# Performance work log

Hardware: AMD Instinct MI355X
Metric: run time of the kernel (lower is better)

## Reference

```python
import jax, jax.numpy as jnp
import numpy as np

B, T, D, H, HF, L, NL = 8, 512, 1024, 16, 4096, 4, 128
HD = D // H  # head dim = 64


def rel_pos_embed(seq_len, dim):
    # Relative sinusoidal embeddings for positions -seq_len .. seq_len-1 (TENER / fairseq style)
    half = dim // 2
    freq = jnp.exp(jnp.arange(half, dtype=jnp.float32) * (-np.log(10000.0) / (half - 1)))
    pos = jnp.arange(-seq_len, seq_len, dtype=jnp.float32)[:, None] * freq[None, :]
    return jnp.concatenate([jnp.sin(pos), jnp.cos(pos)], axis=1)  # (2T, dim)


def layer_norm(x, g, b, eps=1e-5):
    m = jnp.mean(x, axis=-1, keepdims=True)
    v = jnp.mean((x - m) ** 2, axis=-1, keepdims=True)
    return (x - m) * jax.lax.rsqrt(v + eps) * g + b


def rel_attention(x, mask, qv_w, r_r, r_w, pos):
    # x: (B,T,D); qv_w: (D,2D); r_r,r_w: (H,HD); pos: (2T,HD)
    q, v = jnp.split(x @ qv_w, 2, axis=-1)
    q = q.reshape(B, T, H, HD).transpose(0, 2, 1, 3)  # bhqd
    k = x.reshape(B, T, H, HD).transpose(0, 2, 1, 3)  # key is raw input per head (TENER)
    v = v.reshape(B, T, H, HD).transpose(0, 2, 1, 3)
    AC = jnp.einsum('bhqd,bhkd->bhqk', q + r_r[:, None, :], k)
    # B term + D term over all 2T relative positions, then shift: BD[q,k] = BDf[q, T + k - q]
    BDf = jnp.einsum('bhqd,ld->bhql', q, pos) + jnp.einsum('hd,ld->hl', r_w, pos)[None, :, None, :]
    idx = T + jnp.arange(T)[None, :] - jnp.arange(T)[:, None]  # (T,T), values in [1, 2T-1]
    BD = jnp.take_along_axis(BDf, idx[None, None], axis=3)  # (B,H,T,T)
    scores = (AC + BD) / np.float32(np.sqrt(HD))
    scores = jnp.where(mask[:, None, None, :], scores, jnp.float32(-1e9))
    attn = jax.nn.softmax(scores, axis=-1)
    out = jnp.einsum('bhqk,bhkd->bhqd', attn, v)
    return out.transpose(0, 2, 1, 3).reshape(B, T, D)


def setup_inputs() -> dict:
    key = jax.random.key(0)
    ks = jax.random.split(key, 8)
    s = 0.02
    return {
        'x': jax.random.normal(ks[0], (B, T, D), jnp.float32),
        'mask': jnp.ones((B, T), dtype=bool),
        'qv_w': jax.random.normal(ks[1], (L, D, 2 * D), jnp.float32) * s,
        'r_r_bias': jax.random.normal(ks[2], (L, H, HD), jnp.float32) * s,
        'r_w_bias': jax.random.normal(ks[3], (L, H, HD), jnp.float32) * s,
        'ln1_g': jnp.ones((L, D), jnp.float32), 'ln1_b': jnp.zeros((L, D), jnp.float32),
        'w1': jax.random.normal(ks[4], (L, D, HF), jnp.float32) * s, 'b1': jnp.zeros((L, HF), jnp.float32),
        'w2': jax.random.normal(ks[5], (L, HF, D), jnp.float32) * s, 'b2': jnp.zeros((L, D), jnp.float32),
        'ln2_g': jnp.ones((L, D), jnp.float32), 'ln2_b': jnp.zeros((L, D), jnp.float32),
        'cls_w': jax.random.normal(ks[6], (D, NL), jnp.float32) * s, 'cls_b': jnp.zeros((NL,), jnp.float32),
    }


def reference(x, mask, qv_w, r_r_bias, r_w_bias, ln1_g, ln1_b, w1, b1, w2, b2, ln2_g, ln2_b, cls_w, cls_b):
    pos = rel_pos_embed(T, HD)  # (2T, HD)
    h = x
    for l in range(L):  # post-norm relative transformer layer
        h = layer_norm(h + rel_attention(h, mask, qv_w[l], r_r_bias[l], r_w_bias[l], pos), ln1_g[l], ln1_b[l])
        ff = jax.nn.leaky_relu(h @ w1[l] + b1[l]) @ w2[l] + b2[l]
        h = layer_norm(h + ff, ln2_g[l], ln2_b[l])
    return h @ cls_w + cls_b  # logits (B,T,NL)
```

## Files before the change

### kernel.cpp

```cpp
#include <hip/hip_runtime.h>
#include <math.h>

namespace {

constexpr int B = 8, T = 512, D = 1024, H = 16, HD = 64, HF = 4096, L = 4, NL = 128;

typedef _Float16 half8 __attribute__((ext_vector_type(8)));
typedef _Float16 half4 __attribute__((ext_vector_type(4)));
typedef float f32x4 __attribute__((ext_vector_type(4)));

__device__ __forceinline__ void gload16(const void* g, void* l) {
  __builtin_amdgcn_global_load_lds(
      (const __attribute__((address_space(1))) void*)g,
      (__attribute__((address_space(3))) void*)l, 16, 0, 0);
}

__device__ __forceinline__ void stage_half(const _Float16* g0,
                                           const _Float16* g1, char* dst) {
  gload16(g0, dst);
  gload16(g1, dst + 8192);
}

template <int OUT16, int ACT, int HASBIAS>
__global__ __launch_bounds__(256) void gemm_f16(
    const _Float16* __restrict__ A, const _Float16* __restrict__ Bt,
    const float* __restrict__ bias, void* __restrict__ Cout,
    int M, int N, int K) {
  (void)M;
  __shared__ __align__(16) _Float16 Alds[128 * 32];
  __shared__ __align__(16) _Float16 Blds[128 * 32];
  const int t = threadIdx.x;
  const int lane = t & 63;
  const int m0 = blockIdx.y * 128, n0 = blockIdx.x * 128;
  const int wm = (t >> 7) * 64;
  const int wn = ((t >> 6) & 1) * 64;
  f32x4 acc[4][4] = {};
  const int r0 = t >> 2, kc0 = (t & 3) * 8;
  const int r1 = (t + 256) >> 2, kc1 = (t & 3) * 8;
  _Float16* al0 = &Alds[(t & 192) * 8];
  _Float16* al1 = &Alds[(256 + (t & 192)) * 8];
  _Float16* bl0 = &Blds[(t & 192) * 8];
  _Float16* bl1 = &Blds[(256 + (t & 192)) * 8];
  const _Float16* Ar0 = A + (size_t)(m0 + r0) * K + kc0;
  const _Float16* Ar1 = A + (size_t)(m0 + r1) * K + kc1;
  const _Float16* Br0 = Bt + (size_t)(n0 + r0) * K + kc0;
  const _Float16* Br1 = Bt + (size_t)(n0 + r1) * K + kc1;
  const int ml = lane & 15, qd = lane >> 4;

  for (int kk = 0; kk < K; kk += 32) {
    gload16(Ar0 + kk, al0);
    gload16(Ar1 + kk, al1);
    gload16(Br0 + kk, bl0);
    gload16(Br1 + kk, bl1);
    __syncthreads();
    half8 a[4], b[4];
#pragma unroll
    for (int i = 0; i < 4; i++)
      a[i] = *(const half8*)&Alds[(wm + i * 16 + ml) * 32 + qd * 8];
#pragma unroll
    for (int j = 0; j < 4; j++)
      b[j] = *(const half8*)&Blds[(wn + j * 16 + ml) * 32 + qd * 8];
#pragma unroll
    for (int i = 0; i < 4; i++)
#pragma unroll
      for (int j = 0; j < 4; j++)
        acc[i][j] =
            __builtin_amdgcn_mfma_f32_16x16x32_f16(a[i], b[j], acc[i][j], 0, 0, 0);
    __syncthreads();
  }
#pragma unroll
  for (int j = 0; j < 4; j++) {
    const int col = n0 + wn + j * 16 + ml;
    const float bv = HASBIAS ? bias[col] : 0.f;
#pragma unroll
    for (int i = 0; i < 4; i++) {
      const int rowb = m0 + wm + i * 16 + qd * 4;
#pragma unroll
      for (int r = 0; r < 4; r++) {
        float v = acc[i][j][r] + bv;
        if (ACT == 1) v = v >= 0.f ? v : 0.01f * v;
        if (OUT16)
          ((_Float16*)Cout)[(size_t)(rowb + r) * N + col] = (_Float16)v;
        else
          ((float*)Cout)[(size_t)(rowb + r) * N + col] = v;
      }
    }
  }
}

template <int ACT, int HASBIAS, int NSPLIT>
__global__ __launch_bounds__(512, 2) void gemm256(
    const _Float16* __restrict__ A, const _Float16* __restrict__ Bt,
    const float* __restrict__ bias, _Float16* C0, _Float16* C1,
    _Float16* C2, _Float16* C3, int N, int K) {
  __shared__ __align__(16) char smem[131072];
  const int t = threadIdx.x;
  const int wave = t >> 6, lane = t & 63, ml = lane & 15, qd = lane >> 4;
  const int wr = wave >> 2, wc = wave & 3;
  const int n0 = blockIdx.x * 256, m0 = blockIdx.y * 256;
  const int z = (NSPLIT > 1) ? (int)blockIdx.z : 0;
  const int Kc = K / NSPLIT;
  const int NT = Kc >> 6;
  const size_t kz = (size_t)z * Kc;
  const int l0 = t >> 3;
  const int uu = (t & 7) ^ (l0 & 7);
  const int rs = ((uu >> 2) << 7) | l0;
  const _Float16* aS0 = A + (size_t)(m0 + rs) * K + kz + (uu & 3) * 8;
  const _Float16* aS1 = aS0 + (size_t)64 * K;
  const _Float16* bS0 = Bt + (size_t)(n0 + rs) * K + kz + (uu & 3) * 8;
  const _Float16* bS1 = bS0 + (size_t)64 * K;
  char* const wdst = smem + (wave << 10);
  int offA[8], offB[4];
#pragma unroll
  for (int m = 0; m < 8; m++) {
    const int r = wr * 128 + m * 16 + ml;
    offA[m] = (r & 127) * 128 + (((((r >> 7) << 2) | qd) ^ (r & 7)) << 4);
  }
#pragma unroll
  for (int n = 0; n < 4; n++) {
    const int r = wc * 64 + n * 16 + ml;
    offB[n] = (r & 127) * 128 + (((((r >> 7) << 2) | qd) ^ (r & 7)) << 4);
  }
  f32x4 acc[8][4] = {};
  stage_half(aS0, aS1, wdst);
  stage_half(bS0, bS1, wdst + 16384);
  stage_half(aS0 + 32, aS1 + 32, wdst + 32768);
  stage_half(bS0 + 32, bS1 + 32, wdst + 49152);
  stage_half(aS0 + 64, aS1 + 64, wdst + 65536);
  stage_half(bS0 + 64, bS1 + 64, wdst + 81920);
  asm volatile("s_waitcnt vmcnt(4)" ::: "memory");
  __builtin_amdgcn_s_barrier();

  for (int kt = 0; kt < NT; ++kt) {
    const int pb = kt & 1;
    char* const cur = smem + pb * 65536;
    char* const wcur = cur + (wave << 10);
    char* const wnxt = smem + (pb ^ 1) * 65536 + (wave << 10);
    const int kb = kt * 64;
    half8 a[4], b[4];
#pragma unroll
    for (int n = 0; n < 4; n++) b[n] = *(const half8*)(cur + 16384 + offB[n]);
#pragma unroll
    for (int i = 0; i < 4; i++) a[i] = *(const half8*)(cur + offA[i]);
    if (kt + 1 < NT) stage_half(aS0 + kb + 96, aS1 + kb + 96, wnxt + 32768);
    __builtin_amdgcn_s_barrier();
    asm volatile("s_waitcnt lgkmcnt(0)" ::: "memory");
    __builtin_amdgcn_sched_barrier(0);
    __builtin_amdgcn_s_setprio(1);
#pragma unroll
    for (int i = 0; i < 4; i++)
#pragma unroll
      for (int n = 0; n < 4; n++)
        acc[i][n] =
            __builtin_amdgcn_mfma_f32_16x16x32_f16(a[i], b[n], acc[i][n], 0, 0, 0);
    __builtin_amdgcn_s_setprio(0);
    __builtin_amdgcn_s_barrier();
#pragma unroll
    for (int i = 0; i < 4; i++) a[i] = *(const half8*)(cur + offA[4 + i]);
    if (kt + 1 < NT) stage_half(bS0 + kb + 96, bS1 + kb + 96, wnxt + 49152);
    __builtin_amdgcn_s_barrier();
    asm volatile("s_waitcnt lgkmcnt(0)" ::: "memory");
    __builtin_amdgcn_sched_barrier(0);
    __builtin_amdgcn_s_setprio(1);
#pragma unroll
    for (int i = 0; i < 4; i++)
#pragma unroll
      for (int n = 0; n < 4; n++)
        acc[4 + i][n] = __builtin_amdgcn_mfma_f32_16x16x32_f16(a[i], b[n],
                                                               acc[4 + i][n], 0, 0, 0);
    __builtin_amdgcn_s_setprio(0);
    __builtin_amdgcn_s_barrier();
    if (kt == NT - 1) asm volatile("s_waitcnt vmcnt(0)" ::: "memory");
#pragma unroll
    for (int n = 0; n < 4; n++) b[n] = *(const half8*)(cur + 49152 + offB[n]);
#pragma unroll
    for (int i = 0; i < 4; i++) a[i] = *(const half8*)(cur + 32768 + offA[i]);
    if (kt + 2 < NT) stage_half(aS0 + kb + 128, aS1 + kb + 128, wcur);
    __builtin_amdgcn_s_barrier();
    asm volatile("s_waitcnt lgkmcnt(0)" ::: "memory");
    __builtin_amdgcn_sched_barrier(0);
    __builtin_amdgcn_s_setprio(1);
#pragma unroll
    for (int i = 0; i < 4; i++)
#pragma unroll
      for (int n = 0; n < 4; n++)
        acc[i][n] =
            __builtin_amdgcn_mfma_f32_16x16x32_f16(a[i], b[n], acc[i][n], 0, 0, 0);
    __builtin_amdgcn_s_setprio(0);
    __builtin_amdgcn_s_barrier();
#pragma unroll
    for (int i = 0; i < 4; i++) a[i] = *(const half8*)(cur + 32768 + offA[4 + i]);
    if (kt + 2 < NT) stage_half(bS0 + kb + 128, bS1 + kb + 128, wcur + 16384);
    __builtin_amdgcn_s_barrier();
    asm volatile("s_waitcnt lgkmcnt(0)" ::: "memory");
    __builtin_amdgcn_sched_barrier(0);
    __builtin_amdgcn_s_setprio(1);
#pragma unroll
    for (int i = 0; i < 4; i++)
#pragma unroll
      for (int n = 0; n < 4; n++)
        acc[4 + i][n] = __builtin_amdgcn_mfma_f32_16x16x32_f16(a[i], b[n],
                                                               acc[4 + i][n], 0, 0, 0);
    __builtin_amdgcn_s_setprio(0);
    asm volatile("s_waitcnt vmcnt(4)" ::: "memory");
    __builtin_amdgcn_s_barrier();
  }
  _Float16* Cz = (NSPLIT == 1) ? C0 : (z == 0 ? C0 : z == 1 ? C1 : z == 2 ? C2 : C3);
#pragma unroll
  for (int n = 0; n < 4; n++) {
    const int col = n0 + wc * 64 + n * 16 + ml;
    const float bv = HASBIAS ? bias[col] : 0.f;
#pragma unroll
    for (int m = 0; m < 8; m++) {
      const int rowb = m0 + wr * 128 + m * 16 + qd * 4;
#pragma unroll
      for (int r = 0; r < 4; r++) {
        float v = acc[m][n][r] + bv;
        if (ACT == 1) v = v >= 0.f ? v : 0.01f * v;
        Cz[(size_t)(rowb + r) * N + col] = (_Float16)v;
      }
    }
  }
}

__global__ __launch_bounds__(256) void wcvt_t(
    const float* __restrict__ W, _Float16* __restrict__ Wt, int K, int N) {
  __shared__ float tile[64][65];
  const int t = threadIdx.x;
  const int n0 = blockIdx.x * 64, k0 = blockIdx.y * 64;
#pragma unroll
  for (int i = 0; i < 4; i++) {
    int idx = t + i * 256;
    int r = idx >> 4, c = (idx & 15) * 4;
    float4 v = *(const float4*)(W + (size_t)(k0 + r) * N + n0 + c);
    tile[r][c + 0] = v.x;
    tile[r][c + 1] = v.y;
    tile[r][c + 2] = v.z;
    tile[r][c + 3] = v.w;
  }
  __syncthreads();
#pragma unroll
  for (int i = 0; i < 4; i++) {
    int idx = t + i * 256;
    int n = idx >> 4, kc = (idx & 15) * 4;
    half4 o;
    o.x = (_Float16)tile[kc + 0][n];
    o.y = (_Float16)tile[kc + 1][n];
    o.z = (_Float16)tile[kc + 2][n];
    o.w = (_Float16)tile[kc + 3][n];
    *(half4*)(Wt + (size_t)(n0 + n) * K + k0 + kc) = o;
  }
}

__global__ __launch_bounds__(256) void cvt_dual(
    const float* __restrict__ X, float* __restrict__ Y,
    _Float16* __restrict__ Y16) {
  const size_t idx = (size_t)blockIdx.x * 256 + threadIdx.x;
  float4 v = ((const float4*)X)[idx];
  ((float4*)Y)[idx] = v;
  half4 o;
  o.x = (_Float16)v.x; o.y = (_Float16)v.y;
  o.z = (_Float16)v.z; o.w = (_Float16)v.w;
  ((half4*)Y16)[idx] = o;
}

__global__ __launch_bounds__(256) void build_trig(
    float* __restrict__ trig, _Float16* __restrict__ trig16) {
  const int idx = blockIdx.x * 256 + threadIdx.x;
  const int tpos = idx >> 5, i = idx & 31;
  const float f = expf(-0.2971077539347156f * (float)i);
  float sp, cp;
  sincosf((float)tpos * f, &sp, &cp);
  trig[tpos * 64 + i] = sp;
  trig[tpos * 64 + 32 + i] = cp;
  trig16[tpos * 64 + i] = (_Float16)sp;
  trig16[tpos * 64 + 32 + i] = (_Float16)cp;
}

__global__ __launch_bounds__(256) void vtrans(const _Float16* __restrict__ qv16,
                                              _Float16* __restrict__ vT) {
  __shared__ _Float16 tile[64][72];
  const int t = threadIdx.x;
  const int bh = blockIdx.x >> 3, tt = blockIdx.x & 7;
  const int bb = bh >> 4, hh = bh & 15;
  const int t0 = tt * 64;
#pragma unroll
  for (int i = 0; i < 2; i++) {
    int f = i * 256 + t;
    int r = f >> 3, c8 = (f & 7) * 8;
    *(half8*)&tile[r][c8] = *(const half8*)(qv16 +
        (size_t)(bb * T + t0 + r) * (2 * D) + D + hh * HD + c8);
  }
  __syncthreads();
#pragma unroll
  for (int i = 0; i < 2; i++) {
    int f = i * 256 + t;
    int d = f >> 3, c8 = (f & 7) * 8;
    half8 o8;
#pragma unroll
    for (int j = 0; j < 8; j++) o8[j] = tile[c8 + j][d];
    *(half8*)(vT + ((size_t)bh * HD + d) * T + t0 + c8) = o8;
  }
}

__global__ __launch_bounds__(256) void attn_mfma(
    const _Float16* __restrict__ qv16, const _Float16* __restrict__ h16,
    const _Float16* __restrict__ vT, const _Float16* __restrict__ trig16,
    const float* __restrict__ trig, const float* __restrict__ rr,
    const float* __restrict__ rw, float* __restrict__ out) {
  constexpr int CK = 64;
  __shared__ __align__(16) char smem[59392];
  _Float16* QeL = (_Float16*)smem;
  _Float16* KcL = (_Float16*)smem;
  _Float16* KtL = (_Float16*)(smem + 8192);
  _Float16* VtL = (_Float16*)(smem + 16384);
  const int t = threadIdx.x;
  const int wave = t >> 6, lane = t & 63;
  const int ml = lane & 15, qd = lane >> 4;
  _Float16* PL = (_Float16*)(smem + 24576) + wave * (32 * 136);
  const int bh = blockIdx.x >> 2, qt = blockIdx.x & 3;
  const int hh = bh & 15, bb = bh >> 4;
  const int q0 = qt * 128;

  {
    const int row = t >> 1, ch = t & 1;
    const _Float16* q16row =
        qv16 + (size_t)(bb * T + q0 + row) * (2 * D) + hh * HD;
    const float* rrh = rr + hh * HD;
    const float* rwh = rw + hh * HD;
    _Float16* dst = QeL + row * 136 + ch * 64;
    if (ch == 0) {
#pragma unroll
      for (int c8 = 0; c8 < 8; c8++) {
        half8 qv = *(const half8*)(q16row + c8 * 8);
        half8 o8;
#pragma unroll
        for (int j = 0; j < 8; j++)
          o8[j] = (_Float16)(((float)qv[j] + rrh[c8 * 8 + j]) * 0.125f);
        *(half8*)(dst + c8 * 8) = o8;
      }
    } else {
      const float* tr = trig + (q0 + row) * 64;
#pragma unroll
      for (int i8 = 0; i8 < 4; i8++) {
        half8 qu = *(const half8*)(q16row + i8 * 8);
        half8 qw = *(const half8*)(q16row + 32 + i8 * 8);
        half8 so, co;
#pragma unroll
        for (int j = 0; j < 8; j++) {
          int i = i8 * 8 + j;
          float u = (float)qu[j] + rwh[i];
          float w = (float)qw[j] + rwh[i + 32];
          float sp = tr[i], cp = tr[32 + i];
          so[j] = (_Float16)((u * cp + w * sp) * 0.125f);
          co[j] = (_Float16)((w * cp - u * sp) * 0.125f);
        }
        *(half8*)(dst + i8 * 8) = so;
        *(half8*)(dst + 32 + i8 * 8) = co;
      }
    }
  }
  __syncthreads();
  const int wq0 = wave * 32;
  half8 aq[2][4];
#pragma unroll
  for (int mt = 0; mt < 2; mt++)
#pragma unroll
    for (int s = 0; s < 4; s++)
      aq[mt][s] =
          *(const half8*)&QeL[(wq0 + mt * 16 + ml) * 136 + s * 32 + qd * 8];
  __syncthreads();

  float m8[2][4], l8[2][4];
  f32x4 o[2][4] = {};
#pragma unroll
  for (int mt = 0; mt < 2; mt++)
#pragma unroll
    for (int r = 0; r < 4; r++) { m8[mt][r] = -INFINITY; l8[mt][r] = 0.f; }

  const _Float16* hkb = h16 + (size_t)bb * T * D + hh * HD;
  const _Float16* vtb = vT + (size_t)bh * HD * T;

  for (int kc = 0; kc < T / CK; kc++) {
#pragma unroll
    for (int is = 0; is < 2; is++) {
      int f = (is * 4 + wave) * 64 + lane;
      int r = f >> 3, cg = (f ^ r) & 7;
      gload16(hkb + (size_t)(kc * CK + r) * D + cg * 8,
              (char*)KcL + (is * 4 + wave) * 1024);
      gload16(trig16 + (size_t)(kc * CK + r) * 64 + cg * 8,
              (char*)KtL + (is * 4 + wave) * 1024);
      gload16(vtb + (size_t)r * T + kc * CK + cg * 8,
              (char*)VtL + (is * 4 + wave) * 1024);
    }
    __syncthreads();
    f32x4 s[2][4] = {};
#pragma unroll
    for (int step = 0; step < 4; step++) {
      const _Float16* kl = (step < 2) ? KcL : KtL;
      const int cr = (step & 1) * 4 + qd;
#pragma unroll
      for (int kt = 0; kt < 4; kt++) {
        const int rk = kt * 16 + ml;
        half8 b = *(const half8*)&kl[rk * 64 + ((cr ^ rk) & 7) * 8];
        s[0][kt] = __builtin_amdgcn_mfma_f32_16x16x32_f16(aq[0][step], b,
                                                          s[0][kt], 0, 0, 0);
        s[1][kt] = __builtin_amdgcn_mfma_f32_16x16x32_f16(aq[1][step], b,
                                                          s[1][kt], 0, 0, 0);
      }
    }
#pragma unroll
    for (int mt = 0; mt < 2; mt++) {
#pragma unroll
      for (int r = 0; r < 4; r++) {
        float mx = fmaxf(fmaxf(s[mt][0][r], s[mt][1][r]),
                         fmaxf(s[mt][2][r], s[mt][3][r]));
        mx = fmaxf(mx, __shfl_xor(mx, 1));
        mx = fmaxf(mx, __shfl_xor(mx, 2));
        mx = fmaxf(mx, __shfl_xor(mx, 4));
        mx = fmaxf(mx, __shfl_xor(mx, 8));
        const float mnew = fmaxf(m8[mt][r], mx);
        const float alpha = __expf(m8[mt][r] - mnew);
        float psum = 0.f;
#pragma unroll
        for (int kt = 0; kt < 4; kt++) {
          float p = __expf(s[mt][kt][r] - mnew);
          psum += p;
          PL[(mt * 16 + qd * 4 + r) * 136 + kt * 16 + ml] = (_Float16)p;
        }
        psum += __shfl_xor(psum, 1);
        psum += __shfl_xor(psum, 2);
        psum += __shfl_xor(psum, 4);
        psum += __shfl_xor(psum, 8);
        m8[mt][r] = mnew;
        l8[mt][r] = l8[mt][r] * alpha + psum;
#pragma unroll
        for (int dt = 0; dt < 4; dt++) o[mt][dt][r] *= alpha;
      }
    }
#pragma unroll
    for (int s2 = 0; s2 < 2; s2++) {
      half8 bv[4];
      const int cr = s2 * 4 + qd;
#pragma unroll
      for (int dt = 0; dt < 4; dt++) {
        const int rd = dt * 16 + ml;
        bv[dt] = *(const half8*)&VtL[rd * 64 + ((cr ^ rd) & 7) * 8];
      }
#pragma unroll
      for (int mt = 0; mt < 2; mt++) {
        half8 ap = *(const half8*)&PL[(mt * 16 + ml) * 136 + s2 * 32 + qd * 8];
#pragma unroll
        for (int dt = 0; dt < 4; dt++)
          o[mt][dt] = __builtin_amdgcn_mfma_f32_16x16x32_f16(ap, bv[dt],
                                                             o[mt][dt], 0, 0, 0);
      }
    }
    __syncthreads();
  }
  float* ob = out + ((size_t)bb * T + q0 + wq0) * D + hh * HD;
#pragma unroll
  for (int mt = 0; mt < 2; mt++)
#pragma unroll
    for (int r = 0; r < 4; r++) {
      const float inv = 1.f / l8[mt][r];
      const int qrow = mt * 16 + qd * 4 + r;
#pragma unroll
      for (int dt = 0; dt < 4; dt++)
        ob[(size_t)qrow * D + dt * 16 + ml] = o[mt][dt][r] * inv;
    }
}

__global__ __launch_bounds__(256) void resid_ln(
    const float* __restrict__ X, const float* __restrict__ R,
    const float* __restrict__ g, const float* __restrict__ bta,
    float* __restrict__ Y, _Float16* __restrict__ Y16) {
  const int row = blockIdx.x, t = threadIdx.x;
  const size_t base = (size_t)row * D + t * 4;
  float4 x = *(const float4*)(X + base);
  float4 r = *(const float4*)(R + base);
  float4 v;
  v.x = x.x + r.x; v.y = x.y + r.y; v.z = x.z + r.z; v.w = x.w + r.w;
  float s = v.x + v.y + v.z + v.w;
  float s2 = v.x * v.x + v.y * v.y + v.z * v.z + v.w * v.w;
#pragma unroll
  for (int off = 32; off > 0; off >>= 1) {
    s += __shfl_down(s, off);
    s2 += __shfl_down(s2, off);
  }
  __shared__ float red[8];
  const int lane = t & 63, wid = t >> 6;
  if (lane == 0) { red[wid] = s; red[4 + wid] = s2; }
  __syncthreads();
  s = red[0] + red[1] + red[2] + red[3];
  s2 = red[4] + red[5] + red[6] + red[7];
  const float mean = s * (1.f / D);
  const float var = s2 * (1.f / D) - mean * mean;
  const float rstd = rsqrtf(var + 1e-5f);
  float4 gv = *(const float4*)(g + t * 4);
  float4 bv = *(const float4*)(bta + t * 4);
  float4 o;
  o.x = (v.x - mean) * rstd * gv.x + bv.x;
  o.y = (v.y - mean) * rstd * gv.y + bv.y;
  o.z = (v.z - mean) * rstd * gv.z + bv.z;
  o.w = (v.w - mean) * rstd * gv.w + bv.w;
  *(float4*)(Y + base) = o;
  half4 o16;
  o16.x = (_Float16)o.x; o16.y = (_Float16)o.y;
  o16.z = (_Float16)o.z; o16.w = (_Float16)o.w;
  ((half4*)Y16)[(size_t)row * (D / 4) + t] = o16;
}

__global__ __launch_bounds__(256) void resid_ln_ff4(
    const float* __restrict__ X, const _Float16* P0, const _Float16* P1,
    const _Float16* P2, const _Float16* P3, const float* __restrict__ b2,
    const float* __restrict__ g, const float* __restrict__ bta,
    float* __restrict__ Y, _Float16* Y16) {
  const int row = blockIdx.x, t = threadIdx.x;
  const size_t base = (size_t)row * D + t * 4;
  float4 x = *(const float4*)(X + base);
  half4 p0 = *(const half4*)(P0 + base);
  half4 p1 = *(const half4*)(P1 + base);
  half4 p2 = *(const half4*)(P2 + base);
  half4 p3 = *(const half4*)(P3 + base);
  float4 bb = *(const float4*)(b2 + t * 4);
  float4 v;
  v.x = x.x + (float)p0.x + (float)p1.x + (float)p2.x + (float)p3.x + bb.x;
  v.y = x.y + (float)p0.y + (float)p1.y + (float)p2.y + (float)p3.y + bb.y;
  v.z = x.z + (float)p0.z + (float)p1.z + (float)p2.z + (float)p3.z + bb.z;
  v.w = x.w + (float)p0.w + (float)p1.w + (float)p2.w + (float)p3.w + bb.w;
  float s = v.x + v.y + v.z + v.w;
  float s2 = v.x * v.x + v.y * v.y + v.z * v.z + v.w * v.w;
#pragma unroll
  for (int off = 32; off > 0; off >>= 1) {
    s += __shfl_down(s, off);
    s2 += __shfl_down(s2, off);
  }
  __shared__ float red[8];
  const int lane = t & 63, wid = t >> 6;
  if (lane == 0) { red[wid] = s; red[4 + wid] = s2; }
  __syncthreads();
  s = red[0] + red[1] + red[2] + red[3];
  s2 = red[4] + red[5] + red[6] + red[7];
  const float mean = s * (1.f / D);
  const float var = s2 * (1.f / D) - mean * mean;
  const float rstd = rsqrtf(var + 1e-5f);
  float4 gv = *(const float4*)(g + t * 4);
  float4 bv = *(const float4*)(bta + t * 4);
  float4 o;
  o.x = (v.x - mean) * rstd * gv.x + bv.x;
  o.y = (v.y - mean) * rstd * gv.y + bv.y;
  o.z = (v.z - mean) * rstd * gv.z + bv.z;
  o.w = (v.w - mean) * rstd * gv.w + bv.w;
  *(float4*)(Y + base) = o;
  half4 o16;
  o16.x = (_Float16)o.x; o16.y = (_Float16)o.y;
  o16.z = (_Float16)o.z; o16.w = (_Float16)o.w;
  ((half4*)Y16)[(size_t)row * (D / 4) + t] = o16;
}

}

extern "C" void kernel_launch(void* const* d_in, const int* in_sizes, int n_in,
                              void* d_out, int out_size, void* d_ws, size_t ws_size,
                              hipStream_t stream) {
  (void)in_sizes; (void)n_in; (void)out_size; (void)ws_size;
  const float* x    = (const float*)d_in[0];
  const float* qv_w = (const float*)d_in[2];
  const float* r_r  = (const float*)d_in[3];
  const float* r_w  = (const float*)d_in[4];
  const float* ln1g = (const float*)d_in[5];
  const float* ln1b = (const float*)d_in[6];
  const float* w1   = (const float*)d_in[7];
  const float* b1   = (const float*)d_in[8];
  const float* w2   = (const float*)d_in[9];
  const float* b2   = (const float*)d_in[10];
  const float* ln2g = (const float*)d_in[11];
  const float* ln2b = (const float*)d_in[12];
  const float* clsw = (const float*)d_in[13];
  const float* clsb = (const float*)d_in[14];
  float* out = (float*)d_out;
  char* ws = (char*)d_ws;
  const int M = B * T;
  float*     hbuf  = (float*)(ws + 0);
  float*     tmp   = (float*)(ws + 16777216);
  _Float16*  qv16  = (_Float16*)(ws + 33554432);
  _Float16*  vT16  = (_Float16*)(ws + 50331648);
  _Float16*  ff1h  = (_Float16*)(ws + 33554432);
  _Float16*  h16   = (_Float16*)(ws + 67108864);
  _Float16*  wqv   = (_Float16*)(ws + 75497472);
  _Float16*  w1t   = (_Float16*)(ws + 79691776);
  _Float16*  w2t   = (_Float16*)(ws + 88080384);
  float*     trig  = (float*)(ws + 96468992);
  _Float16*  trig16= (_Float16*)(ws + 96600064);
  _Float16*  fp0 = (_Float16*)(ws + 16777216);
  _Float16*  fp1 = (_Float16*)(ws + 16777216 + 8388608);
  _Float16*  fp2 = (_Float16*)(ws + 75497472);
  _Float16*  fp3 = (_Float16*)(ws + 67108864);
  _Float16*  clsw16 = (_Float16*)(ws + 33554432);

  cvt_dual<<<M * D / 1024, 256, 0, stream>>>(x, hbuf, h16);
  build_trig<<<64, 256, 0, stream>>>(trig, trig16);

  for (int l = 0; l < L; l++) {
    wcvt_t<<<dim3(2 * D / 64, D / 64), 256, 0, stream>>>(
        qv_w + (size_t)l * D * 2 * D, wqv, D, 2 * D);
    wcvt_t<<<dim3(HF / 64, D / 64), 256, 0, stream>>>(
        w1 + (size_t)l * D * HF, w1t, D, HF);
    wcvt_t<<<dim3(D / 64, HF / 64), 256, 0, stream>>>(
        w2 + (size_t)l * HF * D, w2t, HF, D);
    gemm256<0, 0, 1><<<dim3(2 * D / 256, M / 256), 512, 0, stream>>>(
        h16, wqv, nullptr, qv16, nullptr, nullptr, nullptr, 2 * D, D);
    vtrans<<<B * H * 8, 256, 0, stream>>>(qv16, vT16);
    attn_mfma<<<B * H * 4, 256, 0, stream>>>(
        qv16, h16, vT16, trig16, trig,
        r_r + (size_t)l * H * HD, r_w + (size_t)l * H * HD, tmp);
    resid_ln<<<M, 256, 0, stream>>>(hbuf, tmp,
        ln1g + (size_t)l * D, ln1b + (size_t)l * D, hbuf, h16);
    gemm256<1, 1, 1><<<dim3(HF / 256, M / 256), 512, 0, stream>>>(
        h16, w1t, b1 + (size_t)l * HF, ff1h, nullptr, nullptr, nullptr,
        HF, D);
    gemm256<0, 0, 4><<<dim3(D / 256, M / 256, 4), 512, 0, stream>>>(
        ff1h, w2t, nullptr, fp0, fp1, fp2, fp3, D, HF);
    resid_ln_ff4<<<M, 256, 0, stream>>>(hbuf, fp0, fp1, fp2, fp3,
        b2 + (size_t)l * D, ln2g + (size_t)l * D, ln2b + (size_t)l * D,
        hbuf, h16);
  }
  wcvt_t<<<dim3(NL / 64, D / 64), 256, 0, stream>>>(clsw, clsw16, D, NL);
  gemm_f16<0, 0, 1><<<dim3(NL / 128, M / 128), 256, 0, stream>>>(
      h16, clsw16, clsb, out, M, NL, D);
}
```

Measured before the change: 1.049 ms.

## Pipeline K/V staging in attention and use lazy softmax rescale with MFMA row sums

Splits K and V staging in the attention kernel so the next chunk's K tiles load while softmax and P·V run, and V loads after P·V, with manual vmcnt waits and raw barriers in place of __syncthreads. Only rescales the running max and output when some row's max rises by more than a threshold (checked wave-wide). Row sums come from an extra MFMA of P against a ones vector, which removes the shuffle reductions. The hand-counted waitcnt values and the barrier ordering are fragile, and the lazy rescale risks fp16 range issues in P if the threshold is too loose.

```diff
diff --git a/kernel.cpp b/kernel.cpp
--- a/kernel.cpp
+++ b/kernel.cpp
@@ -309,6 +309,7 @@
     const float* __restrict__ trig, const float* __restrict__ rr,
     const float* __restrict__ rw, float* __restrict__ out) {
   constexpr int CK = 64;
+  constexpr int NC = T / CK;
   __shared__ __align__(16) char smem[59392];
   _Float16* QeL = (_Float16*)smem;
   _Float16* KcL = (_Float16*)smem;
@@ -371,17 +372,22 @@
           *(const half8*)&QeL[(wq0 + mt * 16 + ml) * 136 + s * 32 + qd * 8];
   __syncthreads();
 
-  float m8[2][4], l8[2][4];
+  float m8[2][4];
+  f32x4 lacc[2] = {};
   f32x4 o[2][4] = {};
 #pragma unroll
   for (int mt = 0; mt < 2; mt++)
 #pragma unroll
-    for (int r = 0; r < 4; r++) { m8[mt][r] = -INFINITY; l8[mt][r] = 0.f; }
+    for (int r = 0; r < 4; r++) m8[mt][r] = -INFINITY;
+
+  half8 vone;
+#pragma unroll
+  for (int j = 0; j < 8; j++) vone[j] = (_Float16)1.f;
 
   const _Float16* hkb = h16 + (size_t)bb * T * D + hh * HD;
   const _Float16* vtb = vT + (size_t)bh * HD * T;
 
-  for (int kc = 0; kc < T / CK; kc++) {
+  auto stageK = [&](int kc) {
 #pragma unroll
     for (int is = 0; is < 2; is++) {
       int f = (is * 4 + wave) * 64 + lane;
@@ -390,10 +396,24 @@
               (char*)KcL + (is * 4 + wave) * 1024);
       gload16(trig16 + (size_t)(kc * CK + r) * 64 + cg * 8,
               (char*)KtL + (is * 4 + wave) * 1024);
+    }
+  };
+  auto stageV = [&](int kc) {
+#pragma unroll
+    for (int is = 0; is < 2; is++) {
+      int f = (is * 4 + wave) * 64 + lane;
+      int r = f >> 3, cg = (f ^ r) & 7;
       gload16(vtb + (size_t)r * T + kc * CK + cg * 8,
               (char*)VtL + (is * 4 + wave) * 1024);
     }
-    __syncthreads();
+  };
+
+  stageK(0);
+  stageV(0);
+  asm volatile("s_waitcnt vmcnt(2)" ::: "memory");
+  __builtin_amdgcn_s_barrier();
+
+  for (int kc = 0; kc < NC; kc++) {
     f32x4 s[2][4] = {};
 #pragma unroll
     for (int step = 0; step < 4; step++) {
@@ -409,8 +429,15 @@
                                                           s[1][kt], 0, 0, 0);
       }
     }
-#pragma unroll
-    for (int mt = 0; mt < 2; mt++) {
+    __builtin_amdgcn_s_barrier();
+    asm volatile("" ::: "memory");
+    __builtin_amdgcn_sched_barrier(0);
+    if (kc + 1 < NC) stageK(kc + 1);
+
+    float mx8[2][4];
+    float need = 0.f;
+#pragma unroll
+    for (int mt = 0; mt < 2; mt++)
 #pragma unroll
       for (int r = 0; r < 4; r++) {
         float mx = fmaxf(fmaxf(s[mt][0][r], s[mt][1][r]),
@@ -419,51 +446,72 @@
         mx = fmaxf(mx, __shfl_xor(mx, 2));
         mx = fmaxf(mx, __shfl_xor(mx, 4));
         mx = fmaxf(mx, __shfl_xor(mx, 8));
-        const float mnew = fmaxf(m8[mt][r], mx);
-        const float alpha = __expf(m8[mt][r] - mnew);
-        float psum = 0.f;
-#pragma unroll
-        for (int kt = 0; kt < 4; kt++) {
-          float p = __expf(s[mt][kt][r] - mnew);
-          psum += p;
-          PL[(mt * 16 + qd * 4 + r) * 136 + kt * 16 + ml] = (_Float16)p;
+        mx8[mt][r] = mx;
+        if (mx > m8[mt][r] + 5.5f) need = 1.f;
+      }
+    if (__any(need > 0.f)) {
+#pragma unroll
+      for (int mt = 0; mt < 2; mt++)
+#pragma unroll
+        for (int r = 0; r < 4; r++) {
+          const float mnew = fmaxf(m8[mt][r], mx8[mt][r]);
+          const float alpha = __expf(m8[mt][r] - mnew);
+          m8[mt][r] = mnew;
+          lacc[mt][r] *= alpha;
+#pragma unroll
+          for (int dt = 0; dt < 4; dt++) o[mt][dt][r] *= alpha;
         }
-        psum += __shfl_xor(psum, 1);
-        psum += __shfl_xor(psum, 2);
-        psum += __shfl_xor(psum, 4);
-        psum += __shfl_xor(psum, 8);
-        m8[mt][r] = mnew;
-        l8[mt][r] = l8[mt][r] * alpha + psum;
-#pragma unroll
-        for (int dt = 0; dt < 4; dt++) o[mt][dt][r] *= alpha;
-      }
-    }
+    }
+#pragma unroll
+    for (int mt = 0; mt < 2; mt++)
+#pragma unroll
+      for (int r = 0; r < 4; r++)
+#pragma unroll
+        for (int kt = 0; kt < 4; kt++)
+          PL[(mt * 16 + qd * 4 + r) * 136 + kt * 16 + ml] =
+              (_Float16)__expf(s[mt][kt][r] - m8[mt][r]);
+
+    if (kc + 1 < NC)
+      asm volatile("s_waitcnt vmcnt(4)" ::: "memory");
+    else
+      asm volatile("s_waitcnt vmcnt(0)" ::: "memory");
+    __builtin_amdgcn_s_barrier();
+
 #pragma unroll
     for (int s2 = 0; s2 < 2; s2++) {
-      half8 bv[4];
+      half8 bvv[4];
       const int cr = s2 * 4 + qd;
 #pragma unroll
       for (int dt = 0; dt < 4; dt++) {
         const int rd = dt * 16 + ml;
-        bv[dt] = *(const half8*)&VtL[rd * 64 + ((cr ^ rd) & 7) * 8];
+        bvv[dt] = *(const half8*)&VtL[rd * 64 + ((cr ^ rd) & 7) * 8];
       }
 #pragma unroll
       for (int mt = 0; mt < 2; mt++) {
         half8 ap = *(const half8*)&PL[(mt * 16 + ml) * 136 + s2 * 32 + qd * 8];
 #pragma unroll
         for (int dt = 0; dt < 4; dt++)
-          o[mt][dt] = __builtin_amdgcn_mfma_f32_16x16x32_f16(ap, bv[dt],
+          o[mt][dt] = __builtin_amdgcn_mfma_f32_16x16x32_f16(ap, bvv[dt],
                                                              o[mt][dt], 0, 0, 0);
-      }
-    }
-    __syncthreads();
+        lacc[mt] = __builtin_amdgcn_mfma_f32_16x16x32_f16(ap, vone,
+                                                          lacc[mt], 0, 0, 0);
+      }
+    }
+    __builtin_amdgcn_s_barrier();
+    asm volatile("" ::: "memory");
+    __builtin_amdgcn_sched_barrier(0);
+    if (kc + 1 < NC) {
+      stageV(kc + 1);
+      asm volatile("s_waitcnt vmcnt(2)" ::: "memory");
+    }
+    __builtin_amdgcn_s_barrier();
   }
   float* ob = out + ((size_t)bb * T + q0 + wq0) * D + hh * HD;
 #pragma unroll
   for (int mt = 0; mt < 2; mt++)
 #pragma unroll
     for (int r = 0; r < 4; r++) {
-      const float inv = 1.f / l8[mt][r];
+      const float inv = 1.f / lacc[mt][r];
       const int qrow = mt * 16 + qd * 4 + r;
 #pragma unroll
       for (int dt = 0; dt < 4; dt++)
```

Result: faster. 980.8 us (-6.5%).
